# Performance work log

Measured on AMD Instinct MI355X. Metric: run time of the kernel, lower is better.

## Reference

```python
import jax, jax.numpy as jnp
import numpy as np
from jax import lax

# FPN anchor layout: 800x800 image, 3 anchors/loc, strides 4,8,16,32,64
LEVEL_ANCHORS = [120000, 30000, 7500, 1875, 507]
PRE_NMS_TOP_N = 1000   # per level (test mode)
POST_NMS_TOP_N = 1000
NMS_THRESH = 0.7
MIN_SIZE = 1e-3


def setup_inputs() -> dict:
    key = jax.random.key(0)
    k1, k2, k3, k4 = jax.random.split(key, 4)
    A = sum(LEVEL_ANCHORS)
    bs = 2
    predicts = jax.random.normal(k1, (bs, A, 4), jnp.float32) * 0.1
    objectness = jax.random.normal(k2, (bs, A, 1), jnp.float32)
    cxy = jax.random.uniform(k3, (A, 2), jnp.float32, 0.0, 800.0)
    wh = jax.random.uniform(k4, (A, 2), jnp.float32, 16.0, 128.0)
    anchors = jnp.concatenate([cxy - 0.5 * wh, cxy + 0.5 * wh], axis=-1)
    valid_size = jnp.full((bs, 2), 800.0, jnp.float32)  # (w, h) per image
    return {"predicts": predicts, "objectness": objectness,
            "anchors": anchors, "valid_size": valid_size}


def _decode(predicts, anchors):
    # BoxCoder.decoder with weights [1,1,1,1]
    awh = anchors[:, 2:] - anchors[:, :2]          # [A,2]
    axy = anchors[:, :2] + 0.5 * awh               # [A,2]
    xy = axy + predicts[..., :2] * awh             # [bs,A,2] center
    wh = jnp.exp(predicts[..., 2:]) * awh          # [bs,A,2]
    x1y1 = xy - 0.5 * wh
    return jnp.concatenate([x1y1, x1y1 + wh], axis=-1)  # [bs,A,4]


def _per_level_topk_idx(scores):
    # scores: [bs, A] -> concat of per-level top-k indices (global anchor ids)
    idx_list, offset = [], 0
    for n in LEVEL_ANCHORS:
        k = min(PRE_NMS_TOP_N, n)
        _, top = lax.top_k(scores[:, offset:offset + n], k)
        idx_list.append(top + offset)
        offset += n
    return jnp.concatenate(idx_list, axis=1)  # [bs, K]


def _nms_keep(boxes, valid, thresh):
    # boxes sorted by score desc; returns boolean keep mask (sequential NMS)
    x1, y1, x2, y2 = boxes[:, 0], boxes[:, 1], boxes[:, 2], boxes[:, 3]
    area = (x2 - x1) * (y2 - y1)
    xx1 = jnp.maximum(x1[:, None], x1[None, :])
    yy1 = jnp.maximum(y1[:, None], y1[None, :])
    xx2 = jnp.minimum(x2[:, None], x2[None, :])
    yy2 = jnp.minimum(y2[:, None], y2[None, :])
    inter = jnp.maximum(xx2 - xx1, 0.0) * jnp.maximum(yy2 - yy1, 0.0)
    iou = inter / (area[:, None] + area[None, :] - inter + 1e-9)
    sup = iou > thresh                                   # [N,N]
    N = boxes.shape[0]
    ar = jnp.arange(N)

    def body(i, keep):
        suppressed = jnp.any((ar < i) & keep & sup[i])
        return keep.at[i].set(keep[i] & ~suppressed)

    return lax.fori_loop(0, N, body, valid)


def _filter_image(boxes, scores, lvls, wh):
    # boxes [K,4], scores [K], lvls [K] int, wh [2]=(w,h)
    w, h = wh[0], wh[1]
    x1 = jnp.clip(boxes[:, 0], 0.0, w)
    y1 = jnp.clip(boxes[:, 1], 0.0, h)
    x2 = jnp.clip(boxes[:, 2], 0.0, w)
    y2 = jnp.clip(boxes[:, 3], 0.0, h)
    boxes = jnp.stack([x1, y1, x2, y2], axis=-1)
    valid = (x2 - x1 > MIN_SIZE) & (y2 - y1 > MIN_SIZE)
    s = jnp.where(valid, scores, -jnp.inf)
    order = jnp.argsort(-s)
    boxes, s, lvls, valid = boxes[order], s[order], lvls[order], valid[order]
    # batched_nms: offset each level into a disjoint coordinate range
    max_coord = lax.stop_gradient(jnp.max(boxes)) + 1.0
    off = lvls.astype(boxes.dtype) * max_coord
    keep = _nms_keep(lax.stop_gradient(boxes) + off[:, None], valid, NMS_THRESH)
    # take first POST_NMS_TOP_N kept (boxes are score-sorted)
    rank = jnp.cumsum(keep) - 1
    slot = jnp.where(keep & (rank < POST_NMS_TOP_N), rank, POST_NMS_TOP_N)
    out_b = jnp.zeros((POST_NMS_TOP_N + 1, 4), boxes.dtype).at[slot].set(boxes)[:POST_NMS_TOP_N]
    out_s = jnp.zeros((POST_NMS_TOP_N + 1,), s.dtype).at[slot].set(
        jnp.where(keep, s, 0.0))[:POST_NMS_TOP_N]
    return out_b, out_s


def reference(predicts, objectness, anchors, valid_size):
    bs = predicts.shape[0]
    proposals = _decode(predicts, anchors)            # [bs,A,4]
    scores = objectness[..., 0]                       # [bs,A]
    idx = _per_level_topk_idx(scores)                 # [bs,K]
    bidx = jnp.arange(bs)[:, None]
    boxes = proposals[bidx, idx]                      # [bs,K,4]
    sc = scores[bidx, idx]                            # [bs,K]
    levels_all = jnp.concatenate(
        [jnp.full((n,), i, jnp.int32) for i, n in enumerate(LEVEL_ANCHORS)])
    lvl = levels_all[idx]                             # [bs,K]
    final_boxes, final_scores = jax.vmap(_filter_image)(boxes, sc, lvl, valid_size)
    return final_boxes, final_scores
```

## Files before the change

kernel.cpp:

```cpp
#include <hip/hip_runtime.h>

typedef unsigned int u32;
typedef unsigned long long u64;

#define A_TOT    159882
#define BS       2
#define KTOP     1000
#define CAND_CAP 4096
#define HB       4096
#define ABLK     4096
#define NBH      40
#define EPT      16

static const size_t HIST12_OFF   = 0;
static const size_t CUT_OFF      = 131072;
static const size_t CCNT_OFF     = 131104;
static const size_t MAXC_OFF     = 131136;
static const size_t NV_OFF       = 131144;
static const size_t CHUNKANY_OFF = 131200;
static const size_t ZERO_END     = 132480;
static const size_t CAND_OFF     = 132480;
static const size_t LKEY2_OFF    = 394624;
static const size_t LBOX_OFF     = 476544;
static const size_t LSC_OFF      = 640384;
static const size_t RANK_OFF     = 681344;
static const size_t MASK_OFF     = 759168;

__device__ __forceinline__ int level_of(int a) {
  if (a < 120000) return 0;
  if (a < 150000) return 1;
  if (a < 157500) return 2;
  if (a < 159375) return 3;
  return 4;
}

__device__ __forceinline__ u32 dkey(float s) {
  u32 b = __float_as_uint(s);
  return (b & 0x80000000u) ? b : (~b & 0x7FFFFFFFu);
}
__device__ __forceinline__ float dkey_inv(u32 d) {
  u32 b = (d & 0x80000000u) ? d : (~d & 0x7FFFFFFFu);
  return __uint_as_float(b);
}

__device__ __forceinline__ void decode_clip(const float* __restrict__ pred,
                                            const float* __restrict__ anch,
                                            const float* __restrict__ vs,
                                            int b, int a,
                                            float& x1c, float& y1c, float& x2c, float& y2c,
                                            bool& valid) {
  const float* pp = pred + ((size_t)b * A_TOT + (size_t)a) * 4;
  const float* aa = anch + (size_t)a * 4;
  float ax1 = aa[0], ay1 = aa[1], ax2 = aa[2], ay2 = aa[3];
  float px = pp[0], py = pp[1], pw = pp[2], ph = pp[3];
  float aw  = __fsub_rn(ax2, ax1);
  float ah  = __fsub_rn(ay2, ay1);
  float acx = __fadd_rn(ax1, __fmul_rn(0.5f, aw));
  float acy = __fadd_rn(ay1, __fmul_rn(0.5f, ah));
  float cx  = __fadd_rn(acx, __fmul_rn(px, aw));
  float cy  = __fadd_rn(acy, __fmul_rn(py, ah));
  float w   = __fmul_rn(expf(pw), aw);
  float h   = __fmul_rn(expf(ph), ah);
  float x1  = __fsub_rn(cx, __fmul_rn(0.5f, w));
  float y1  = __fsub_rn(cy, __fmul_rn(0.5f, h));
  float x2  = __fadd_rn(x1, w);
  float y2  = __fadd_rn(y1, h);
  float Wv = vs[b * 2 + 0], Hv = vs[b * 2 + 1];
  x1c = fminf(fmaxf(x1, 0.0f), Wv);
  y1c = fminf(fmaxf(y1, 0.0f), Hv);
  x2c = fminf(fmaxf(x2, 0.0f), Wv);
  y2c = fminf(fmaxf(y2, 0.0f), Hv);
  valid = (__fsub_rn(x2c, x1c) > 0.001f) && (__fsub_rn(y2c, y1c) > 0.001f);
}

__device__ __forceinline__ void bitonic_u64(u64* arr, int N, int t, int nt) {
  for (int k = 2; k <= N; k <<= 1) {
    for (int j = k >> 1; j > 0; j >>= 1) {
      __syncthreads();
      for (int i = t; i < N; i += nt) {
        int ixj = i ^ j;
        if (ixj > i) {
          u64 x = arr[i], y = arr[ixj];
          bool up = ((i & k) == 0);
          if (up ? (x > y) : (x < y)) { arr[i] = y; arr[ixj] = x; }
        }
      }
    }
  }
  __syncthreads();
}

__device__ __forceinline__ u64 shfl_xor_u64(u64 x, int lanemask) {
  u32 lo = (u32)x, hi = (u32)(x >> 32);
  lo = (u32)__shfl_xor((int)lo, lanemask);
  hi = (u32)__shfl_xor((int)hi, lanemask);
  return ((u64)hi << 32) | (u64)lo;
}

__device__ __forceinline__ u64* regsort2048x(u64 v[2], int tid, u64* bufA, u64* bufB) {
  u64* bufs[2] = {bufA, bufB};
  int cur = 0;
  for (int k = 2; k <= 2048; k <<= 1) {
    for (int j = k >> 1; j > 0; j >>= 1) {
      if (j == 1) {
        bool up = (((2 * tid) & k) == 0);
        u64 a = v[0], b2 = v[1];
        bool sw = up ? (a > b2) : (a < b2);
        if (sw) { v[0] = b2; v[1] = a; }
      } else if (j <= 64) {
        int dl = j >> 1;
        bool up = (((2 * tid) & k) == 0);
        bool low = ((tid & dl) == 0);
        bool keepmin = (low == up);
#pragma unroll
        for (int e = 0; e < 2; ++e) {
          u64 o = shfl_xor_u64(v[e], dl);
          v[e] = keepmin ? (v[e] < o ? v[e] : o) : (v[e] > o ? v[e] : o);
        }
      } else {
        u64* B = bufs[cur]; cur ^= 1;
        B[2 * tid] = v[0]; B[2 * tid + 1] = v[1];
        __syncthreads();
#pragma unroll
        for (int e = 0; e < 2; ++e) {
          int i = 2 * tid + e, p = i ^ j;
          u64 o = B[p];
          bool up = ((i & k) == 0);
          bool keepmin = ((i < p) == up);
          v[e] = keepmin ? (v[e] < o ? v[e] : o) : (v[e] > o ? v[e] : o);
        }
      }
    }
  }
  u64* B = bufs[cur];
  B[2 * tid] = v[0]; B[2 * tid + 1] = v[1];
  __syncthreads();
  return B;
}

__global__ void k_zero(char* __restrict__ ws) {
  size_t i = (size_t)blockIdx.x * blockDim.x + threadIdx.x;
  if (i * 4 < ZERO_END) ((u32*)ws)[i] = 0u;
}

__global__ void k_hist12(const float* __restrict__ obj, char* __restrict__ ws) {
  __shared__ u32 h[2 * HB];
  int tid = threadIdx.x;
  int b = blockIdx.x / NBH, loc = blockIdx.x % NBH;
  int start = loc * ABLK;
  int l0 = level_of(start);
  if (l0 >= 4) return;
  for (int i = tid; i < 2 * HB; i += 256) h[i] = 0u;
  __syncthreads();
  for (int it = 0; it < EPT; ++it) {
    int a = start + it * 256 + tid;
    if (a < A_TOT) {
      int l = level_of(a);
      if (l < 4) {
        u32 d = dkey(obj[(size_t)b * A_TOT + a]);
        atomicAdd(&h[(u32)(l - l0) * HB + (d >> 20)], 1u);
      }
    }
  }
  __syncthreads();
  int lend = level_of(min(start + ABLK - 1, A_TOT - 1));
  int nseg = ((l0 + 1 <= lend) && (l0 + 1 < 4)) ? 2 : 1;
  for (int s = 0; s < nseg; ++s) {
    u32* gh = (u32*)(ws + HIST12_OFF) + (size_t)(b * 4 + l0 + s) * HB;
    for (int i = tid; i < HB; i += 256) {
      u32 v = h[s * HB + i];
      if (v) atomicAdd(&gh[i], v);
    }
  }
}

__global__ void k_compactsel(const float* __restrict__ obj, char* __restrict__ ws) {
  __shared__ u32 scan[256];
  __shared__ u32 cutv[2];
  __shared__ u32 lcnt[2], gbase[2];
  int tid = threadIdx.x, lane = tid & 63;
  int b = blockIdx.x / NBH, loc = blockIdx.x % NBH;
  int start = loc * ABLK;
  int l0 = level_of(start);
  if (l0 >= 4) return;
  int lend = level_of(min(start + ABLK - 1, A_TOT - 1));
  int nseg = ((l0 + 1 <= lend) && (l0 + 1 < 4)) ? 2 : 1;
  if (tid < 2) lcnt[tid] = 0;
  for (int s = 0; s < nseg; ++s) {
    int seg = b * 4 + l0 + s;
    const u32* gh = (const u32*)(ws + HIST12_OFF) + (size_t)seg * HB;
    u32 vals[16]; u32 acc = 0;
    for (int q = 0; q < 16; ++q) { vals[q] = gh[tid * 16 + q]; acc += vals[q]; }
    __syncthreads();
    scan[tid] = acc; __syncthreads();
    for (int d = 1; d < 256; d <<= 1) {
      u32 x = (tid >= d) ? scan[tid - d] : 0u; __syncthreads();
      scan[tid] += x; __syncthreads();
    }
    u32 incl = scan[tid], prev = incl - acc;
    if (prev < KTOP && incl >= KTOP) {
      u32 run = prev; int cb = HB - 1;
      for (int q = 0; q < 16; ++q) { run += vals[q]; if (run >= KTOP) { cb = tid * 16 + q; break; } }
      cutv[s] = (u32)cb;
      ((u32*)(ws + CUT_OFF))[seg] = (u32)cb;
    }
  }
  __syncthreads();
  u32 dv[EPT], slotv[EPT], passm = 0, sim = 0;
  for (int it = 0; it < EPT; ++it) {
    int a = start + it * 256 + tid;
    bool pass = false; u32 si = 0, d = 0;
    if (a < A_TOT) {
      int l = level_of(a);
      if (l < 4) {
        si = (u32)(l - l0);
        d = dkey(obj[(size_t)b * A_TOT + a]);
        pass = (d >> 20) <= cutv[si];
      }
    }
    dv[it] = d;
    u64 mp = __ballot(pass);
    u64 m1 = __ballot(pass && si == 1);
    u64 m0 = mp & ~m1;
    u32 slot = 0;
    if (m0) {
      int ld = __builtin_ctzll(m0);
      u32 wb = 0;
      if (lane == ld) wb = atomicAdd(&lcnt[0], (u32)__popcll(m0));
      wb = __shfl(wb, ld);
      if (pass && si == 0) slot = wb + (u32)__popcll(m0 & ((1ull << lane) - 1ull));
    }
    if (m1) {
      int ld = __builtin_ctzll(m1);
      u32 wb = 0;
      if (lane == ld) wb = atomicAdd(&lcnt[1], (u32)__popcll(m1));
      wb = __shfl(wb, ld);
      if (pass && si == 1) slot = wb + (u32)__popcll(m1 & ((1ull << lane) - 1ull));
    }
    slotv[it] = slot;
    if (pass) { passm |= 1u << it; if (si) sim |= 1u << it; }
  }
  __syncthreads();
  if (tid < 2)
    gbase[tid] = lcnt[tid] ? atomicAdd((u32*)(ws + CCNT_OFF) + (b * 4 + l0 + tid), lcnt[tid]) : 0u;
  __syncthreads();
  for (int it = 0; it < EPT; ++it) {
    if ((passm >> it) & 1u) {
      int a = start + it * 256 + tid;
      u32 si = (sim >> it) & 1u;
      int seg = b * 4 + l0 + (int)si;
      u32 gslot = gbase[si] + slotv[it];
      if (gslot < CAND_CAP)
        ((u64*)(ws + CAND_OFF))[(size_t)seg * CAND_CAP + gslot] =
            ((u64)dv[it] << 32) | ((u64)(u32)a << 12) | (u64)gslot;
    }
  }
}

__global__ __launch_bounds__(1024)
void k_sortdec(const float* __restrict__ pred, const float* __restrict__ obj,
               const float* __restrict__ anch, const float* __restrict__ vs,
               char* __restrict__ ws) {
  __shared__ u64 bufAB[4096];
  __shared__ float4 dboxS[2048];
  __shared__ float dscS[2048];
  __shared__ u32 validS[2048];
  __shared__ u64 cm[16];
  u64* bufA = bufAB; u64* bufB = bufAB + 2048;
  int tid = threadIdx.x, lane = tid & 63, wv = tid >> 6;
  int P = blockIdx.x, b = P / 5, l = P % 5;
  int n;
  u64* S;
  if (l == 4) {
    n = 507;
    u64 v[2];
#pragma unroll
    for (int e = 0; e < 2; ++e) {
      int idx = 2 * tid + e;
      if (idx < 507) {
        int a = 159375 + idx;
        float sc = obj[(size_t)b * A_TOT + a];
        float x1, y1, x2, y2; bool valid;
        decode_clip(pred, anch, vs, b, a, x1, y1, x2, y2, valid);
        dboxS[idx] = make_float4(x1, y1, x2, y2);
        dscS[idx] = sc;
        validS[idx] = valid ? 1u : 0u;
        v[e] = ((u64)dkey(sc) << 32) | ((u64)(u32)a << 12) | (u64)idx;
      } else v[e] = ~0ull;
    }
    S = regsort2048x(v, tid, bufA, bufB);
  } else {
    n = KTOP;
    int seg = b * 4 + l;
    u32 cnt = min(((const u32*)(ws + CCNT_OFF))[seg], (u32)CAND_CAP);
    const u64* cand = (const u64*)(ws + CAND_OFF) + (size_t)seg * CAND_CAP;
    if (cnt <= 2048) {
      u64 v[2];
#pragma unroll
      for (int e = 0; e < 2; ++e) {
        int idx = 2 * tid + e;
        if (idx < (int)cnt) {
          u64 key = cand[idx];
          int a = (int)((key >> 12) & 0x3FFFFu);
          float x1, y1, x2, y2; bool valid;
          decode_clip(pred, anch, vs, b, a, x1, y1, x2, y2, valid);
          dboxS[idx] = make_float4(x1, y1, x2, y2);
          dscS[idx] = dkey_inv((u32)(key >> 32));
          validS[idx] = valid ? 1u : 0u;
          v[e] = key;
        } else v[e] = ~0ull;
      }
      S = regsort2048x(v, tid, bufA, bufB);
    } else {
      int N = 2048; while (N < (int)cnt) N <<= 1;
      for (int i = tid; i < N; i += 1024) bufAB[i] = (i < (int)cnt) ? cand[i] : ~0ull;
      bitonic_u64(bufAB, N, tid, 1024);
      for (int j = tid; j < KTOP; j += 1024) {
        u64 key = bufAB[j];
        int a = (int)((key >> 12) & 0x3FFFFu);
        float x1, y1, x2, y2; bool valid;
        decode_clip(pred, anch, vs, b, a, x1, y1, x2, y2, valid);
        dboxS[j] = make_float4(x1, y1, x2, y2);
        dscS[j] = dkey_inv((u32)(key >> 32));
        validS[j] = valid ? 1u : 0u;
        bufAB[j] = (key & ~0xFFFull) | (u64)j;
      }
      __syncthreads();
      S = bufAB;
    }
  }
  float m = 0.0f;
  for (int j = tid; j < n; j += 1024) {
    int slot = (int)(S[j] & 0xFFFull);
    float4 bx = dboxS[slot];
    m = fmaxf(m, fmaxf(fmaxf(bx.x, bx.y), fmaxf(bx.z, bx.w)));
  }
  for (int off = 32; off; off >>= 1) m = fmaxf(m, __shfl_xor(m, off));
  if (lane == 0) atomicMax((u32*)(ws + MAXC_OFF) + b, __float_as_uint(m));
  {
    int j = wv * 64 + lane;
    bool val = (j < n) && (validS[(int)(S[j] & 0xFFFull)] != 0u);
    u64 mask = __ballot(val);
    if (lane == 0) cm[wv] = mask;
    __syncthreads();
    int base = 0;
    for (int w2 = 0; w2 < wv; ++w2) base += __popcll(cm[w2]);
    if (val) {
      int r = base + __popcll(mask & ((1ull << lane) - 1ull));
      int slot = (int)(S[j] & 0xFFFull);
      ((u64*)(ws + LKEY2_OFF))[(size_t)P * 1024 + r] = S[j];
      ((float4*)(ws + LBOX_OFF))[(size_t)P * 1024 + r] = dboxS[slot];
      ((float*)(ws + LSC_OFF))[(size_t)P * 1024 + r] = dscS[slot];
    }
    if (tid == 0) {
      int tot = 0;
      for (int w2 = 0; w2 < 16; ++w2) tot += __popcll(cm[w2]);
      ((u32*)(ws + NV_OFF))[P] = (u32)tot;
    }
  }
}

__device__ __forceinline__ int lbound(const u64* __restrict__ arr, int n, u64 key) {
  int lo = 0, hi = n;
  while (lo < hi) { int mid = (lo + hi) >> 1; if (arr[mid] < key) lo = mid + 1; else hi = mid; }
  return lo;
}

__global__ void k_maskrank(char* __restrict__ ws) {
  __shared__ float4 boxS[1024];
  __shared__ float  areaS[1024];
  int tid = threadIdx.x, bid = blockIdx.x;
  int P = bid >> 6, rblk = bid & 63;
  int b = P / 5, l = P % 5;
  int n = (int)((const u32*)(ws + NV_OFF))[P];
  float M = __uint_as_float(((const u32*)(ws + MAXC_OFF))[b]);
  float maxc = __fadd_rn(M, 1.0f);
  float off = __fmul_rn((float)l, maxc);
  const float4* lbox = (const float4*)(ws + LBOX_OFF) + (size_t)P * 1024;
  for (int i = tid; i < n; i += 256) {
    float4 bx = lbox[i];
    bx.x = __fadd_rn(bx.x, off); bx.y = __fadd_rn(bx.y, off);
    bx.z = __fadd_rn(bx.z, off); bx.w = __fadd_rn(bx.w, off);
    boxS[i] = bx;
    areaS[i] = __fmul_rn(__fsub_rn(bx.z, bx.x), __fsub_rn(bx.w, bx.y));
  }
  {
    int e = rblk * 16 + tid;
    if (tid < 16 && e < n) {
      const u64* lkey = (const u64*)(ws + LKEY2_OFF);
      const u32* nvp = (const u32*)(ws + NV_OFF);
      u64 key = lkey[(size_t)P * 1024 + e];
      const u64* base[4];
      int lo[4], hi[4], q2 = 0;
      for (int l2 = 0; l2 < 5; ++l2) {
        if (l2 == l) continue;
        base[q2] = lkey + (size_t)(b * 5 + l2) * 1024;
        lo[q2] = 0; hi[q2] = (int)nvp[b * 5 + l2];
        ++q2;
      }
      for (int step = 0; step < 11; ++step) {
#pragma unroll
        for (int q = 0; q < 4; ++q) {
          if (lo[q] < hi[q]) {
            int mid = (lo[q] + hi[q]) >> 1;
            u64 v = base[q][mid];
            if (v < key) lo[q] = mid + 1; else hi[q] = mid;
          }
        }
      }
      ((u32*)(ws + RANK_OFF))[(size_t)P * 1024 + e] =
          (u32)(e + lo[0] + lo[1] + lo[2] + lo[3]);
    }
  }
  __syncthreads();
  int i = rblk * 16 + (tid >> 4);
  int w = tid & 15;
  int W = (n + 63) >> 6;
  if (i >= n || w >= W) return;
  float4 bi = boxS[i];
  float ai = areaS[i];
  u64 word = 0;
  int j0 = w << 6;
  int jn = min(64, n - j0);
  if (jn == 64) {
#pragma unroll 4
    for (int t2 = 0; t2 < 64; ++t2) {
      int jj = (t2 + w) & 63;
      float4 bj = boxS[j0 + jj];
      float xx1 = fmaxf(bi.x, bj.x);
      float yy1 = fmaxf(bi.y, bj.y);
      float xx2 = fminf(bi.z, bj.z);
      float yy2 = fminf(bi.w, bj.w);
      float iw = fmaxf(__fsub_rn(xx2, xx1), 0.0f);
      float ih = fmaxf(__fsub_rn(yy2, yy1), 0.0f);
      float inter = __fmul_rn(iw, ih);
      float den = __fadd_rn(__fsub_rn(__fadd_rn(ai, areaS[j0 + jj]), inter), 1e-9f);
      float iou = __fdiv_rn(inter, den);
      if (iou > 0.7f) word |= (1ull << jj);
    }
  } else {
    for (int jj = 0; jj < jn; ++jj) {
      float4 bj = boxS[j0 + jj];
      float xx1 = fmaxf(bi.x, bj.x);
      float yy1 = fmaxf(bi.y, bj.y);
      float xx2 = fminf(bi.z, bj.z);
      float yy2 = fminf(bi.w, bj.w);
      float iw = fmaxf(__fsub_rn(xx2, xx1), 0.0f);
      float ih = fmaxf(__fsub_rn(yy2, yy1), 0.0f);
      float inter = __fmul_rn(iw, ih);
      float den = __fadd_rn(__fsub_rn(__fadd_rn(ai, areaS[j0 + jj]), inter), 1e-9f);
      float iou = __fdiv_rn(inter, den);
      if (iou > 0.7f) word |= (1ull << jj);
    }
  }
  if (i >= j0 && i < j0 + 64) word &= ~(1ull << (i - j0));
  ((u64*)(ws + MASK_OFF))[(size_t)P * 16000 + (size_t)i * W + w] = word;
  if (word)
    atomicOr((u64*)(ws + CHUNKANY_OFF) + (size_t)P * 16 + (i >> 6), 1ull << (i & 63));
}

__global__ __launch_bounds__(320)
void k_scanfin(float* __restrict__ out, char* __restrict__ ws) {
  __shared__ u64 keeps[5][16];
  __shared__ u64 kb[80];
  __shared__ u32 sb[128];
  __shared__ u32 pfx[80];
  __shared__ u32 nvs[5];
  int tid = threadIdx.x, w = tid >> 6, lane = tid & 63;
  int b = blockIdx.x;
  for (int i = tid; i < 80; i += 320) kb[i] = 0ull;
  for (int i = tid; i < 4000; i += 320) out[(size_t)b * 4000 + i] = 0.0f;
  for (int i = tid; i < 1000; i += 320) out[8000 + (size_t)b * 1000 + i] = 0.0f;
  if (tid < 5) nvs[tid] = ((const u32*)(ws + NV_OFF))[b * 5 + tid];

  int P = b * 5 + w;
  int n = (int)((const u32*)(ws + NV_OFF))[P];
  int W = (n + 63) >> 6;
  const u64* maskg = (const u64*)(ws + MASK_OFF) + (size_t)P * 16000;
  u64 ca = (lane < 16) ? ((const u64*)(ws + CHUNKANY_OFF))[(size_t)P * 16 + lane] : 0ull;
  u64 dpre[16];
#pragma unroll
  for (int c = 0; c < 16; ++c) {
    int row = (c << 6) + lane;
    dpre[c] = (c < W && row < n) ? maskg[(size_t)row * W + c] : 0ull;
  }
  u64 removed = 0ull, keepw = 0ull;
#pragma unroll
  for (int c = 0; c < 16; ++c) {
    if (c >= W) break;
    int rb = c << 6;
    int rows = min(64, n - rb);
    u64 rowsmask = (rows == 64) ? ~0ull : ((1ull << rows) - 1ull);
    u64 curw = __shfl(removed, c);
    u64 cand = ~curw & rowsmask;
    u64 ca_c = __shfl(ca, c);
    u64 keptbits;
    u64 anyrows = ca_c & cand;
    if (anyrows == 0ull) {
      keptbits = cand;
    } else {
      u64 diag = dpre[c];
      u64 diagnz = __ballot(diag != 0ull) & cand;
      if (diagnz == 0ull) {
        keptbits = cand;
      } else {
        u64 remw = curw | ~rowsmask;
        u64 kept = 0ull;
        int pos = 0;
        u64 work = diagnz;
        while (work) {
          int s = __builtin_ctzll(work); work &= work - 1;
          u64 range = (1ull << s) - (1ull << pos);
          kept |= ~remw & range;
          bool k = ((remw >> s) & 1ull) == 0ull;
          u64 dr = __shfl(diag, s);
          if (k) { kept |= 1ull << s; remw |= dr; }
          pos = s + 1;
        }
        u64 tail = (pos >= 64) ? 0ull : (~0ull << pos);
        kept |= ~remw & tail & rowsmask;
        keptbits = kept;
      }
      u64 todo = keptbits & ca_c;
      while (todo) {
        int r0 = __builtin_ctzll(todo); todo &= todo - 1;
        int r1 = -1, r2 = -1, r3 = -1;
        if (todo) { r1 = __builtin_ctzll(todo); todo &= todo - 1; }
        if (todo) { r2 = __builtin_ctzll(todo); todo &= todo - 1; }
        if (todo) { r3 = __builtin_ctzll(todo); todo &= todo - 1; }
        u64 v0 = 0, v1 = 0, v2 = 0, v3 = 0;
        if (lane < W) {
          v0 = maskg[(size_t)(rb + r0) * W + lane];
          if (r1 >= 0) v1 = maskg[(size_t)(rb + r1) * W + lane];
          if (r2 >= 0) v2 = maskg[(size_t)(rb + r2) * W + lane];
          if (r3 >= 0) v3 = maskg[(size_t)(rb + r3) * W + lane];
        }
        removed |= v0 | v1 | v2 | v3;
      }
    }
    if (lane == c) keepw |= keptbits;
  }
  if (lane < 16) keeps[w][lane] = keepw;
  __syncthreads();

  const u32* rank = (const u32*)(ws + RANK_OFF);
  for (int idx = tid; idx < 5120; idx += 320) {
    int p = idx >> 10, i = idx & 1023;
    if (i < (int)nvs[p] && ((keeps[p][i >> 6] >> (i & 63)) & 1ull)) {
      u32 r = rank[(size_t)(b * 5 + p) * 1024 + i];
      atomicOr(&kb[r >> 6], 1ull << (r & 63));
    }
  }
  __syncthreads();
  if (tid < 128) sb[tid] = (tid < 80) ? (u32)__popcll(kb[tid]) : 0u;
  __syncthreads();
  for (int d = 1; d < 128; d <<= 1) {
    u32 x = (tid < 128 && tid >= d) ? sb[tid - d] : 0u;
    __syncthreads();
    if (tid < 128) sb[tid] += x;
    __syncthreads();
  }
  if (tid < 80) pfx[tid] = sb[tid] - (u32)__popcll(kb[tid]);
  __syncthreads();
  for (int idx = tid; idx < 5120; idx += 320) {
    int p = idx >> 10, i = idx & 1023;
    if (i < (int)nvs[p] && ((keeps[p][i >> 6] >> (i & 63)) & 1ull)) {
      int Pp = b * 5 + p;
      u32 r = rank[(size_t)Pp * 1024 + i];
      u64 word = kb[r >> 6];
      int slot = (int)pfx[r >> 6] + __popcll(word & ((1ull << (r & 63)) - 1ull));
      if (slot < KTOP) {
        float4 bx = ((const float4*)(ws + LBOX_OFF))[(size_t)Pp * 1024 + i];
        float s = ((const float*)(ws + LSC_OFF))[(size_t)Pp * 1024 + i];
        float* ob = out + ((size_t)b * KTOP + slot) * 4;
        ob[0] = bx.x; ob[1] = bx.y; ob[2] = bx.z; ob[3] = bx.w;
        out[8000 + (size_t)b * KTOP + slot] = s;
      }
    }
  }
}

extern "C" void kernel_launch(void* const* d_in, const int* in_sizes, int n_in,
                              void* d_out, int out_size, void* d_ws, size_t ws_size,
                              hipStream_t stream) {
  const float* pred = (const float*)d_in[0];
  const float* obj  = (const float*)d_in[1];
  const float* anch = (const float*)d_in[2];
  const float* vs   = (const float*)d_in[3];
  float* out = (float*)d_out;
  char* ws = (char*)d_ws;
  (void)in_sizes; (void)n_in; (void)out_size; (void)ws_size;

  int gZ = (int)((ZERO_END / 4 + 255) / 256);
  k_zero      <<<gZ,        256, 0, stream>>>(ws);
  k_hist12    <<<BS * NBH,  256, 0, stream>>>(obj, ws);
  k_compactsel<<<BS * NBH,  256, 0, stream>>>(obj, ws);
  k_sortdec   <<<10,       1024, 0, stream>>>(pred, obj, anch, vs, ws);
  k_maskrank  <<<640,       256, 0, stream>>>(ws);
  k_scanfin   <<<2,         320, 0, stream>>>(out, ws);
}
```

Before: 164.3 us.

## Split cut scan, NMS scan, finalize into separate kernels; skip lower-triangle IoU words

Moves the per-segment histogram cutoff scan out of the compaction kernel into its own small kernel, so each of the 80 compaction blocks no longer repeats the prefix scan. The sequential NMS scan moves from a 2-block finalize kernel into a 10-block kernel that first stages the suppression mask in LDS, spreading the work over more CUs and replacing global reads with shared-memory reads. The IoU mask kernel skips word columns below the diagonal, which the scan never reads. The zero kernel is replaced with hipMemsetAsync, and the launch count goes from six to seven.

New measurement: 168.4 us. +2.5%, slower.

```diff
diff --git a/kernel.cpp b/kernel.cpp
--- a/kernel.cpp
+++ b/kernel.cpp
@@ -13,18 +13,19 @@
 #define EPT      16
 
 static const size_t HIST12_OFF   = 0;
-static const size_t CUT_OFF      = 131072;
-static const size_t CCNT_OFF     = 131104;
-static const size_t MAXC_OFF     = 131136;
-static const size_t NV_OFF       = 131144;
+static const size_t CCNT_OFF     = 131072;
+static const size_t MAXC_OFF     = 131104;
+static const size_t NV_OFF       = 131112;
+static const size_t CUTV_OFF     = 131152;
 static const size_t CHUNKANY_OFF = 131200;
-static const size_t ZERO_END     = 132480;
-static const size_t CAND_OFF     = 132480;
-static const size_t LKEY2_OFF    = 394624;
-static const size_t LBOX_OFF     = 476544;
-static const size_t LSC_OFF      = 640384;
-static const size_t RANK_OFF     = 681344;
-static const size_t MASK_OFF     = 759168;
+static const size_t KEEPS_OFF    = 132480;
+static const size_t ZERO_END     = 133760;
+static const size_t CAND_OFF     = 133760;
+static const size_t LKEY2_OFF    = 395904;
+static const size_t LBOX_OFF     = 477824;
+static const size_t LSC_OFF      = 641664;
+static const size_t RANK_OFF     = 682624;
+static const size_t MASK_OFF     = 723584;
 
 __device__ __forceinline__ int level_of(int a) {
   if (a < 120000) return 0;
@@ -138,11 +139,6 @@
   return B;
 }
 
-__global__ void k_zero(char* __restrict__ ws) {
-  size_t i = (size_t)blockIdx.x * blockDim.x + threadIdx.x;
-  if (i * 4 < ZERO_END) ((u32*)ws)[i] = 0u;
-}
-
 __global__ void k_hist12(const float* __restrict__ obj, char* __restrict__ ws) {
   __shared__ u32 h[2 * HB];
   int tid = threadIdx.x;
@@ -174,8 +170,28 @@
   }
 }
 
-__global__ void k_compactsel(const float* __restrict__ obj, char* __restrict__ ws) {
+__global__ __launch_bounds__(256)
+void k_cut(char* __restrict__ ws) {
   __shared__ u32 scan[256];
+  int tid = threadIdx.x;
+  int seg = blockIdx.x;
+  const u32* gh = (const u32*)(ws + HIST12_OFF) + (size_t)seg * HB;
+  u32 vals[16]; u32 acc = 0;
+  for (int q = 0; q < 16; ++q) { vals[q] = gh[tid * 16 + q]; acc += vals[q]; }
+  scan[tid] = acc; __syncthreads();
+  for (int d = 1; d < 256; d <<= 1) {
+    u32 x = (tid >= d) ? scan[tid - d] : 0u; __syncthreads();
+    scan[tid] += x; __syncthreads();
+  }
+  u32 incl = scan[tid], prev = incl - acc;
+  if (prev < KTOP && incl >= KTOP) {
+    u32 run = prev; int cb = HB - 1;
+    for (int q = 0; q < 16; ++q) { run += vals[q]; if (run >= KTOP) { cb = tid * 16 + q; break; } }
+    ((u32*)(ws + CUTV_OFF))[seg] = (u32)cb;
+  }
+}
+
+__global__ void k_compact(const float* __restrict__ obj, char* __restrict__ ws) {
   __shared__ u32 cutv[2];
   __shared__ u32 lcnt[2], gbase[2];
   int tid = threadIdx.x, lane = tid & 63;
@@ -186,25 +202,7 @@
   int lend = level_of(min(start + ABLK - 1, A_TOT - 1));
   int nseg = ((l0 + 1 <= lend) && (l0 + 1 < 4)) ? 2 : 1;
   if (tid < 2) lcnt[tid] = 0;
-  for (int s = 0; s < nseg; ++s) {
-    int seg = b * 4 + l0 + s;
-    const u32* gh = (const u32*)(ws + HIST12_OFF) + (size_t)seg * HB;
-    u32 vals[16]; u32 acc = 0;
-    for (int q = 0; q < 16; ++q) { vals[q] = gh[tid * 16 + q]; acc += vals[q]; }
-    __syncthreads();
-    scan[tid] = acc; __syncthreads();
-    for (int d = 1; d < 256; d <<= 1) {
-      u32 x = (tid >= d) ? scan[tid - d] : 0u; __syncthreads();
-      scan[tid] += x; __syncthreads();
-    }
-    u32 incl = scan[tid], prev = incl - acc;
-    if (prev < KTOP && incl >= KTOP) {
-      u32 run = prev; int cb = HB - 1;
-      for (int q = 0; q < 16; ++q) { run += vals[q]; if (run >= KTOP) { cb = tid * 16 + q; break; } }
-      cutv[s] = (u32)cb;
-      ((u32*)(ws + CUT_OFF))[seg] = (u32)cb;
-    }
-  }
+  if (tid < nseg) cutv[tid] = ((const u32*)(ws + CUTV_OFF))[b * 4 + l0 + tid];
   __syncthreads();
   u32 dv[EPT], slotv[EPT], passm = 0, sim = 0;
   for (int it = 0; it < EPT; ++it) {
@@ -360,12 +358,6 @@
   }
 }
 
-__device__ __forceinline__ int lbound(const u64* __restrict__ arr, int n, u64 key) {
-  int lo = 0, hi = n;
-  while (lo < hi) { int mid = (lo + hi) >> 1; if (arr[mid] < key) lo = mid + 1; else hi = mid; }
-  return lo;
-}
-
 __global__ void k_maskrank(char* __restrict__ ws) {
   __shared__ float4 boxS[1024];
   __shared__ float  areaS[1024];
@@ -416,7 +408,7 @@
   int i = rblk * 16 + (tid >> 4);
   int w = tid & 15;
   int W = (n + 63) >> 6;
-  if (i >= n || w >= W) return;
+  if (i >= n || w >= W || w < (i >> 6)) return;
   float4 bi = boxS[i];
   float ai = areaS[i];
   u64 word = 0;
@@ -459,88 +451,100 @@
     atomicOr((u64*)(ws + CHUNKANY_OFF) + (size_t)P * 16 + (i >> 6), 1ull << (i & 63));
 }
 
+__global__ __launch_bounds__(1024)
+void k_scan(char* __restrict__ ws) {
+  __shared__ u64 maskL[16000];
+  int tid = threadIdx.x, lane = tid & 63;
+  int P = blockIdx.x;
+  int n = (int)((const u32*)(ws + NV_OFF))[P];
+  int W = (n + 63) >> 6;
+  const u64* maskg = (const u64*)(ws + MASK_OFF) + (size_t)P * 16000;
+  int T = n * W;
+  for (int t = tid; t < T; t += 1024) maskL[t] = maskg[t];
+  __syncthreads();
+  if (tid < 64) {
+    u64 ca = (lane < 16) ? ((const u64*)(ws + CHUNKANY_OFF))[(size_t)P * 16 + lane] : 0ull;
+    u64 dpre[16];
+#pragma unroll
+    for (int c = 0; c < 16; ++c) {
+      int row = (c << 6) + lane;
+      dpre[c] = (c < W && row < n) ? maskL[(size_t)row * W + c] : 0ull;
+    }
+    u64 removed = 0ull, keepw = 0ull;
+#pragma unroll
+    for (int c = 0; c < 16; ++c) {
+      if (c >= W) break;
+      int rb = c << 6;
+      int rows = min(64, n - rb);
+      u64 rowsmask = (rows == 64) ? ~0ull : ((1ull << rows) - 1ull);
+      u64 curw = __shfl(removed, c);
+      u64 cand = ~curw & rowsmask;
+      u64 ca_c = __shfl(ca, c);
+      u64 keptbits;
+      u64 anyrows = ca_c & cand;
+      if (anyrows == 0ull) {
+        keptbits = cand;
+      } else {
+        u64 diag = dpre[c];
+        u64 diagnz = __ballot(diag != 0ull) & cand;
+        if (diagnz == 0ull) {
+          keptbits = cand;
+        } else {
+          u64 remw = curw | ~rowsmask;
+          u64 kept = 0ull;
+          int pos = 0;
+          u64 work = diagnz;
+          while (work) {
+            int s = __builtin_ctzll(work); work &= work - 1;
+            u64 range = (1ull << s) - (1ull << pos);
+            kept |= ~remw & range;
+            bool k = ((remw >> s) & 1ull) == 0ull;
+            u64 dr = __shfl(diag, s);
+            if (k) { kept |= 1ull << s; remw |= dr; }
+            pos = s + 1;
+          }
+          u64 tail = (pos >= 64) ? 0ull : (~0ull << pos);
+          kept |= ~remw & tail & rowsmask;
+          keptbits = kept;
+        }
+        u64 todo = keptbits & ca_c;
+        while (todo) {
+          int r0 = __builtin_ctzll(todo); todo &= todo - 1;
+          int r1 = -1, r2 = -1, r3 = -1;
+          if (todo) { r1 = __builtin_ctzll(todo); todo &= todo - 1; }
+          if (todo) { r2 = __builtin_ctzll(todo); todo &= todo - 1; }
+          if (todo) { r3 = __builtin_ctzll(todo); todo &= todo - 1; }
+          u64 v0 = 0, v1 = 0, v2 = 0, v3 = 0;
+          if (lane < W) {
+            v0 = maskL[(size_t)(rb + r0) * W + lane];
+            if (r1 >= 0) v1 = maskL[(size_t)(rb + r1) * W + lane];
+            if (r2 >= 0) v2 = maskL[(size_t)(rb + r2) * W + lane];
+            if (r3 >= 0) v3 = maskL[(size_t)(rb + r3) * W + lane];
+          }
+          removed |= v0 | v1 | v2 | v3;
+        }
+      }
+      if (lane == c) keepw |= keptbits;
+    }
+    if (lane < 16)
+      ((u64*)(ws + KEEPS_OFF))[(size_t)P * 16 + lane] = keepw;
+  }
+}
+
 __global__ __launch_bounds__(320)
-void k_scanfin(float* __restrict__ out, char* __restrict__ ws) {
+void k_fin(float* __restrict__ out, char* __restrict__ ws) {
   __shared__ u64 keeps[5][16];
   __shared__ u64 kb[80];
   __shared__ u32 sb[128];
   __shared__ u32 pfx[80];
   __shared__ u32 nvs[5];
-  int tid = threadIdx.x, w = tid >> 6, lane = tid & 63;
+  int tid = threadIdx.x;
   int b = blockIdx.x;
   for (int i = tid; i < 80; i += 320) kb[i] = 0ull;
   for (int i = tid; i < 4000; i += 320) out[(size_t)b * 4000 + i] = 0.0f;
   for (int i = tid; i < 1000; i += 320) out[8000 + (size_t)b * 1000 + i] = 0.0f;
   if (tid < 5) nvs[tid] = ((const u32*)(ws + NV_OFF))[b * 5 + tid];
-
-  int P = b * 5 + w;
-  int n = (int)((const u32*)(ws + NV_OFF))[P];
-  int W = (n + 63) >> 6;
-  const u64* maskg = (const u64*)(ws + MASK_OFF) + (size_t)P * 16000;
-  u64 ca = (lane < 16) ? ((const u64*)(ws + CHUNKANY_OFF))[(size_t)P * 16 + lane] : 0ull;
-  u64 dpre[16];
-#pragma unroll
-  for (int c = 0; c < 16; ++c) {
-    int row = (c << 6) + lane;
-    dpre[c] = (c < W && row < n) ? maskg[(size_t)row * W + c] : 0ull;
-  }
-  u64 removed = 0ull, keepw = 0ull;
-#pragma unroll
-  for (int c = 0; c < 16; ++c) {
-    if (c >= W) break;
-    int rb = c << 6;
-    int rows = min(64, n - rb);
-    u64 rowsmask = (rows == 64) ? ~0ull : ((1ull << rows) - 1ull);
-    u64 curw = __shfl(removed, c);
-    u64 cand = ~curw & rowsmask;
-    u64 ca_c = __shfl(ca, c);
-    u64 keptbits;
-    u64 anyrows = ca_c & cand;
-    if (anyrows == 0ull) {
-      keptbits = cand;
-    } else {
-      u64 diag = dpre[c];
-      u64 diagnz = __ballot(diag != 0ull) & cand;
-      if (diagnz == 0ull) {
-        keptbits = cand;
-      } else {
-        u64 remw = curw | ~rowsmask;
-        u64 kept = 0ull;
-        int pos = 0;
-        u64 work = diagnz;
-        while (work) {
-          int s = __builtin_ctzll(work); work &= work - 1;
-          u64 range = (1ull << s) - (1ull << pos);
-          kept |= ~remw & range;
-          bool k = ((remw >> s) & 1ull) == 0ull;
-          u64 dr = __shfl(diag, s);
-          if (k) { kept |= 1ull << s; remw |= dr; }
-          pos = s + 1;
-        }
-        u64 tail = (pos >= 64) ? 0ull : (~0ull << pos);
-        kept |= ~remw & tail & rowsmask;
-        keptbits = kept;
-      }
-      u64 todo = keptbits & ca_c;
-      while (todo) {
-        int r0 = __builtin_ctzll(todo); todo &= todo - 1;
-        int r1 = -1, r2 = -1, r3 = -1;
-        if (todo) { r1 = __builtin_ctzll(todo); todo &= todo - 1; }
-        if (todo) { r2 = __builtin_ctzll(todo); todo &= todo - 1; }
-        if (todo) { r3 = __builtin_ctzll(todo); todo &= todo - 1; }
-        u64 v0 = 0, v1 = 0, v2 = 0, v3 = 0;
-        if (lane < W) {
-          v0 = maskg[(size_t)(rb + r0) * W + lane];
-          if (r1 >= 0) v1 = maskg[(size_t)(rb + r1) * W + lane];
-          if (r2 >= 0) v2 = maskg[(size_t)(rb + r2) * W + lane];
-          if (r3 >= 0) v3 = maskg[(size_t)(rb + r3) * W + lane];
-        }
-        removed |= v0 | v1 | v2 | v3;
-      }
-    }
-    if (lane == c) keepw |= keptbits;
-  }
-  if (lane < 16) keeps[w][lane] = keepw;
+  if (tid < 80) keeps[tid >> 4][tid & 15] = ((const u64*)(ws + KEEPS_OFF))[(size_t)b * 80 + tid];
   __syncthreads();
 
   const u32* rank = (const u32*)(ws + RANK_OFF);
@@ -591,11 +595,12 @@
   char* ws = (char*)d_ws;
   (void)in_sizes; (void)n_in; (void)out_size; (void)ws_size;
 
-  int gZ = (int)((ZERO_END / 4 + 255) / 256);
-  k_zero      <<<gZ,        256, 0, stream>>>(ws);
-  k_hist12    <<<BS * NBH,  256, 0, stream>>>(obj, ws);
-  k_compactsel<<<BS * NBH,  256, 0, stream>>>(obj, ws);
-  k_sortdec   <<<10,       1024, 0, stream>>>(pred, obj, anch, vs, ws);
-  k_maskrank  <<<640,       256, 0, stream>>>(ws);
-  k_scanfin   <<<2,         320, 0, stream>>>(out, ws);
-}
+  hipMemsetAsync(ws, 0, ZERO_END, stream);
+  k_hist12  <<<BS * NBH, 256, 0, stream>>>(obj, ws);
+  k_cut     <<<BS * 4,   256, 0, stream>>>(ws);
+  k_compact <<<BS * NBH, 256, 0, stream>>>(obj, ws);
+  k_sortdec <<<10,      1024, 0, stream>>>(pred, obj, anch, vs, ws);
+  k_maskrank<<<640,      256, 0, stream>>>(ws);
+  k_scan    <<<10,      1024, 0, stream>>>(ws);
+  k_fin     <<<2,        320, 0, stream>>>(out, ws);
+}
```
